# Optimization experiments

Hardware: AMD Instinct MI355X
Metric: run time of the kernel (lower is better)

The kernel has to match this reference:

```python
import jax, jax.numpy as jnp
import numpy as np

EMB = 1024
HEADS = 16
HEADSIZE = EMB // HEADS
EPS = 1e-5  # torch LayerNorm default


def _layernorm(x, g, b):
    # normalize over last dim (headsize)
    m = jnp.mean(x, axis=-1, keepdims=True)
    v = jnp.mean((x - m) ** 2, axis=-1, keepdims=True)
    return (x - m) * jax.lax.rsqrt(v + EPS) * g + b


def setup_inputs() -> dict:
    key = jax.random.key(0)
    ks = jax.random.split(key, 6)
    B, T = 4, 2048
    s = 1.0 / np.sqrt(EMB)  # ~ torch Linear init scale
    return {
        "x": jax.random.normal(ks[0], (B, T, EMB), dtype=jnp.float32),
        "Wk": jax.random.normal(ks[1], (EMB, EMB), dtype=jnp.float32) * s,
        "Wq": jax.random.normal(ks[2], (EMB, EMB), dtype=jnp.float32) * s,
        "Wv": jax.random.normal(ks[3], (EMB, EMB), dtype=jnp.float32) * s,
        "Wo": jax.random.normal(ks[4], (EMB, EMB), dtype=jnp.float32) * s,
        "bo": jnp.zeros((EMB,), dtype=jnp.float32),
        "kln_g": jnp.ones((HEADSIZE,), dtype=jnp.float32),
        "kln_b": jnp.zeros((HEADSIZE,), dtype=jnp.float32),
        "qln_g": jnp.ones((HEADSIZE,), dtype=jnp.float32),
        "qln_b": jnp.zeros((HEADSIZE,), dtype=jnp.float32),
    }


def reference(x, Wk, Wq, Wv, Wo, bo, kln_g, kln_b, qln_g, qln_b):
    B, T, E = x.shape
    # projections (torch Linear: y = x @ W.T), split into heads
    k = jnp.einsum("bte,fe->btf", x, Wk).reshape(B, T, HEADS, HEADSIZE)
    q = jnp.einsum("bte,fe->btf", x, Wq).reshape(B, T, HEADS, HEADSIZE)
    v = jnp.einsum("bte,fe->btf", x, Wv).reshape(B, T, HEADS, HEADSIZE)
    # optional per-head layernorm on keys/queries (kqnorm=True)
    k = _layernorm(k, kln_g, kln_b)
    q = _layernorm(q, qln_g, qln_b)
    # note: original scales by emb**-1/4 on each of q and k (total 1/sqrt(emb))
    scale = E ** (-0.25)
    q = q * scale
    k = k * scale
    # full [B, H, T, T] score matrix (faithful to bmm implementation)
    dot = jnp.einsum("bihd,bjhd->bhij", q, k)
    # causal mask: j > i set to -inf (mask_diagonal=False -> offset=1)
    causal = jnp.triu(jnp.ones((T, T), dtype=bool), k=1)
    dot = jnp.where(causal, -jnp.inf, dot)
    att = jax.nn.softmax(dot, axis=-1)
    out = jnp.einsum("bhij,bjhd->bihd", att, v).reshape(B, T, E)
    return jnp.einsum("bte,fe->btf", out, Wo) + bo
```

## Files before the change

### kernel.cpp

```cpp
#include <hip/hip_runtime.h>
#include <hip/hip_bf16.h>
#include <cstdint>

#define EMB 1024
#define HEADS 16
#define HD 64
#define BATCH 4
#define SEQ 2048
#define BT (BATCH*SEQ)
#define LNEPS 1e-5f
#define QK_SCALE 0.17677669529663687f
#define LOG2E 1.4426950408889634f

typedef __bf16 bf16;
typedef __bf16 bf16x8 __attribute__((ext_vector_type(8)));
typedef __bf16 bf16x4 __attribute__((ext_vector_type(4)));
typedef float  f32x4  __attribute__((ext_vector_type(4)));
typedef short  s16x4  __attribute__((ext_vector_type(4)));

typedef const __attribute__((address_space(1))) void* gas_ptr;
typedef __attribute__((address_space(3))) void*       las_ptr;

__device__ __forceinline__ void gld_lds16(const void* g, void* l) {
  __builtin_amdgcn_global_load_lds((gas_ptr)g, (las_ptr)l, 16, 0, 0);
}

__device__ __forceinline__ f32x4 mfma_pv(bf16x4 a, bf16x4 b, f32x4 c) {
  return __builtin_amdgcn_mfma_f32_16x16x16bf16_1k(
      __builtin_bit_cast(s16x4, a), __builtin_bit_cast(s16x4, b), c, 0, 0, 0);
}

__global__ void cvt_f32_bf16(const float* __restrict__ src, bf16* __restrict__ dst, int n4) {
  int i = blockIdx.x * blockDim.x + threadIdx.x;
  if (i >= n4) return;
  float4 f = reinterpret_cast<const float4*>(src)[i];
  bf16x4 o = { (bf16)f.x, (bf16)f.y, (bf16)f.z, (bf16)f.w };
  reinterpret_cast<bf16x4*>(dst)[i] = o;
}

__global__ void cvt_w4(const float* __restrict__ w0, const float* __restrict__ w1,
                       const float* __restrict__ w2, const float* __restrict__ w3,
                       bf16* __restrict__ dst) {
  int i = blockIdx.x * blockDim.x + threadIdx.x;
  int sel = i >> 18;
  int j = i & 262143;
  const float* s = (sel == 0) ? w0 : (sel == 1) ? w1 : (sel == 2) ? w2 : w3;
  float4 f = reinterpret_cast<const float4*>(s)[j];
  bf16x4 o = { (bf16)f.x, (bf16)f.y, (bf16)f.z, (bf16)f.w };
  reinterpret_cast<bf16x4*>(dst)[i] = o;
}

template<int OUTF32>
__global__ __launch_bounds__(256, 2) void gemm_bt(
    const bf16* __restrict__ A, const bf16* __restrict__ Bm,
    bf16* __restrict__ Cb, float* __restrict__ Cf, const float* __restrict__ bias,
    int M, int N, int K)
{
  __shared__ __align__(16) bf16 As[128 * 32];
  __shared__ __align__(16) bf16 Bs[128 * 32];

  const int t    = threadIdx.x;
  const int lane = t & 63;
  const int wave = t >> 6;
  const int q    = lane >> 4;
  const int ln   = lane & 15;
  const int m0   = blockIdx.y * 128;
  const int n0   = blockIdx.x * 128;
  const int wm   = (wave >> 1) * 64;
  const int wn   = (wave & 1) * 64;

  const int r0 = t >> 2;
  const int c0 = (t & 3) << 3;

  f32x4 zero4 = {0.f, 0.f, 0.f, 0.f};
  f32x4 acc[4][4];
#pragma unroll
  for (int i = 0; i < 4; i++)
#pragma unroll
    for (int j = 0; j < 4; j++) acc[i][j] = zero4;

  for (int k0 = 0; k0 < K; k0 += 32) {
    __syncthreads();
    const bf16* ga = A  + (size_t)(m0 + r0) * K + k0 + c0;
    const bf16* gb = Bm + (size_t)(n0 + r0) * K + k0 + c0;
    gld_lds16(ga,                  &As[t * 8]);
    gld_lds16(ga + (size_t)64 * K, &As[t * 8 + 2048]);
    gld_lds16(gb,                  &Bs[t * 8]);
    gld_lds16(gb + (size_t)64 * K, &Bs[t * 8 + 2048]);
    __syncthreads();

    bf16x8 af[4], bfr[4];
#pragma unroll
    for (int mi = 0; mi < 4; mi++)
      af[mi] = *reinterpret_cast<const bf16x8*>(&As[(wm + mi * 16 + ln) * 32 + q * 8]);
#pragma unroll
    for (int ni = 0; ni < 4; ni++)
      bfr[ni] = *reinterpret_cast<const bf16x8*>(&Bs[(wn + ni * 16 + ln) * 32 + q * 8]);
#pragma unroll
    for (int mi = 0; mi < 4; mi++)
#pragma unroll
      for (int ni = 0; ni < 4; ni++)
        acc[mi][ni] = __builtin_amdgcn_mfma_f32_16x16x32_bf16(af[mi], bfr[ni], acc[mi][ni], 0, 0, 0);
  }

#pragma unroll
  for (int mi = 0; mi < 4; mi++) {
#pragma unroll
    for (int ni = 0; ni < 4; ni++) {
#pragma unroll
      for (int r = 0; r < 4; r++) {
        int row = m0 + wm + mi * 16 + q * 4 + r;
        int col = n0 + wn + ni * 16 + ln;
        float v = acc[mi][ni][r];
        if (OUTF32) Cf[(size_t)row * N + col] = v + bias[col];
        else        Cb[(size_t)row * N + col] = (bf16)v;
      }
    }
  }
}

__global__ void ln_kq(const bf16* __restrict__ kqv,
                      bf16* __restrict__ kn, bf16* __restrict__ qn,
                      const float* __restrict__ kg, const float* __restrict__ kb,
                      const float* __restrict__ qg, const float* __restrict__ qb,
                      float kscale, float qscale)
{
  const int t = threadIdx.x;
  const int lr = t & 7;
  const int row = blockIdx.x * 32 + (t >> 3);
  const int tok = row >> 4, h = row & 15;
  const size_t base = (size_t)tok * (3 * EMB) + h * HD + lr * 8;

  bf16x8 vk = *reinterpret_cast<const bf16x8*>(kqv + base);
  bf16x8 vq = *reinterpret_cast<const bf16x8*>(kqv + base + EMB);

  float fk[8], fq[8];
  float sk = 0.f, sq = 0.f, s2k = 0.f, s2q = 0.f;
#pragma unroll
  for (int e = 0; e < 8; e++) {
    fk[e] = (float)vk[e]; fq[e] = (float)vq[e];
    sk += fk[e]; sq += fq[e];
    s2k += fk[e] * fk[e]; s2q += fq[e] * fq[e];
  }
#pragma unroll
  for (int m = 1; m < 8; m <<= 1) {
    sk  += __shfl_xor(sk,  m, 64); sq  += __shfl_xor(sq,  m, 64);
    s2k += __shfl_xor(s2k, m, 64); s2q += __shfl_xor(s2q, m, 64);
  }
  float mk = sk * (1.f / 64.f), mq = sq * (1.f / 64.f);
  float rk = rsqrtf(s2k * (1.f / 64.f) - mk * mk + LNEPS) * kscale;
  float rq = rsqrtf(s2q * (1.f / 64.f) - mq * mq + LNEPS) * qscale;

  bf16x8 ok, oq;
#pragma unroll
  for (int e = 0; e < 8; e++) {
    float gk = kg[lr * 8 + e], bk2 = kb[lr * 8 + e];
    float gq = qg[lr * 8 + e], bq2 = qb[lr * 8 + e];
    ok[e] = (bf16)(((fk[e] - mk) * rk) * gk + bk2 * kscale);
    oq[e] = (bf16)(((fq[e] - mq) * rq) * gq + bq2 * qscale);
  }
  const int b = tok >> 11, tt = tok & 2047;
  const size_t o = ((size_t)(b * HEADS + h) * SEQ + tt) * HD + lr * 8;
  *reinterpret_cast<bf16x8*>(kn + o) = ok;
  *reinterpret_cast<bf16x8*>(qn + o) = oq;
}

__global__ void v_trans(const bf16* __restrict__ in, int ldin, bf16* __restrict__ out)
{
  __shared__ __align__(16) bf16 tile[64][72];
  int bh = blockIdx.y, jt = blockIdx.x;
  int b = bh >> 4, h = bh & 15;
  int t = threadIdx.x;
#pragma unroll
  for (int p = 0; p < 2; p++) {
    int rowj = p * 32 + (t >> 3);
    int cold = (t & 7) << 3;
    bf16x8 v = *reinterpret_cast<const bf16x8*>(
        &in[(size_t)(b * SEQ + jt * 64 + rowj) * ldin + h * HD + cold]);
    *reinterpret_cast<bf16x8*>(&tile[rowj][cold]) = v;
  }
  __syncthreads();
#pragma unroll
  for (int p = 0; p < 2; p++) {
    int rowd = p * 32 + (t >> 3);
    int colj = (t & 7) << 3;
    bf16x8 v;
#pragma unroll
    for (int jj = 0; jj < 8; jj++) v[jj] = tile[colj + jj][rowd];
    *reinterpret_cast<bf16x8*>(&out[((size_t)bh * HD + rowd) * SEQ + jt * 64 + colj]) = v;
  }
}

__global__ __launch_bounds__(256, 8) void attn(
    const bf16* __restrict__ Qn, const bf16* __restrict__ Kn, const bf16* __restrict__ Vt,
    bf16* __restrict__ O)
{
  __shared__ __align__(16) bf16 Ks[32 * 64];
  __shared__ __align__(16) bf16 Vs[64 * 32];

  const int bh = blockIdx.y;
  const int itile = ((int)blockIdx.x + (int)blockIdx.y) & 31;
  const int i0 = itile * 64;
  const int t = threadIdx.x, wave = t >> 6, lane = t & 63;
  const int q = lane >> 4, ln = lane & 15;
  const int qbase = i0 + wave * 16;

  const bf16* qp = Qn + ((size_t)bh * SEQ + qbase + ln) * HD + q * 8;
  bf16x8 qf0 = *reinterpret_cast<const bf16x8*>(qp);
  bf16x8 qf1 = *reinterpret_cast<const bf16x8*>(qp + 32);

  float lrow = 0.f;
  f32x4 zero4 = {0.f, 0.f, 0.f, 0.f};
  f32x4 oacc[4];
#pragma unroll
  for (int md = 0; md < 4; md++) oacc[md] = zero4;

  const int nj = 2 * itile + 2;
  for (int jt = 0; jt < nj; jt++) {
    const int j0 = jt * 32;
    {
      const int u = t * 8;
      const int krow = u >> 6;
      const int kcs = (t & 7) ^ (krow & 7);
      gld_lds16(Kn + ((size_t)bh * SEQ + j0 + krow) * HD + kcs * 8, &Ks[u]);
      const int vd = u >> 5;
      const int vcs = (t & 3) ^ ((vd >> 1) & 3);
      gld_lds16(Vt + ((size_t)bh * HD + vd) * SEQ + j0 + vcs * 8, &Vs[u]);
    }
    __syncthreads();

#pragma unroll
    for (int jb = 0; jb < 2; jb++) {
      if ((j0 + jb * 16) <= (qbase + 15)) {
        const int rowj = jb * 16 + ln;
        bf16x8 kf0 = *reinterpret_cast<const bf16x8*>(&Ks[rowj * 64 + ((q)     ^ (rowj & 7)) * 8]);
        bf16x8 kf1 = *reinterpret_cast<const bf16x8*>(&Ks[rowj * 64 + ((4 + q) ^ (rowj & 7)) * 8]);
        f32x4 z = zero4;
        z = __builtin_amdgcn_mfma_f32_16x16x32_bf16(kf0, qf0, z, 0, 0, 0);
        z = __builtin_amdgcn_mfma_f32_16x16x32_bf16(kf1, qf1, z, 0, 0, 0);
        if (j0 + jb * 16 + 15 > qbase) {
#pragma unroll
          for (int r = 0; r < 4; r++) {
            int jj = j0 + jb * 16 + q * 4 + r;
            int ii = qbase + ln;
            if (jj > ii) z[r] = -1.0e30f;
          }
        }
        float p0 = exp2f(z[0]), p1 = exp2f(z[1]), p2 = exp2f(z[2]), p3 = exp2f(z[3]);
        lrow += (p0 + p1) + (p2 + p3);
        bf16x4 pk = { (bf16)p0, (bf16)p1, (bf16)p2, (bf16)p3 };

#pragma unroll
        for (int md = 0; md < 4; md++) {
          const int rowd = md * 16 + ln;
          const bf16* vp = &Vs[rowd * 32 + (((jb * 2 + (q >> 1)) ^ ((rowd >> 1) & 3)) * 8) + (q & 1) * 4];
          bf16x4 vf = *reinterpret_cast<const bf16x4*>(vp);
          oacc[md] = mfma_pv(vf, pk, oacc[md]);
        }
      }
    }
    __syncthreads();
  }

  float s = lrow;
  s += __shfl_xor(s, 16, 64);
  s += __shfl_xor(s, 32, 64);
  const float inv = 1.f / s;
  const int b = bh >> 4, h = bh & 15;
  const int row = qbase + ln;
#pragma unroll
  for (int md = 0; md < 4; md++) {
    bf16x4 o4 = { (bf16)(oacc[md][0] * inv), (bf16)(oacc[md][1] * inv),
                  (bf16)(oacc[md][2] * inv), (bf16)(oacc[md][3] * inv) };
    int col = h * HD + md * 16 + q * 4;
    *reinterpret_cast<bf16x4*>(&O[(size_t)(b * SEQ + row) * EMB + col]) = o4;
  }
}

extern "C" void kernel_launch(void* const* d_in, const int* in_sizes, int n_in,
                              void* d_out, int out_size, void* d_ws, size_t ws_size,
                              hipStream_t stream)
{
  const float* x   = (const float*)d_in[0];
  const float* Wk  = (const float*)d_in[1];
  const float* Wq  = (const float*)d_in[2];
  const float* Wv  = (const float*)d_in[3];
  const float* Wo  = (const float*)d_in[4];
  const float* bo  = (const float*)d_in[5];
  const float* klg = (const float*)d_in[6];
  const float* klb = (const float*)d_in[7];
  const float* qlg = (const float*)d_in[8];
  const float* qlb = (const float*)d_in[9];
  float* out = (float*)d_out;

  char* ws = (char*)d_ws;
  const size_t OFF_XB  = 0;
  const size_t OFF_WB  = OFF_XB  + (size_t)BT * EMB * 2;
  const size_t OFF_KQV = OFF_WB  + (size_t)4 * EMB * EMB * 2;
  const size_t OFF_KN  = OFF_KQV + (size_t)BT * 3 * EMB * 2;
  const size_t OFF_QN  = OFF_KN  + (size_t)BT * EMB * 2;
  const size_t OFF_VT  = OFF_QN  + (size_t)BT * EMB * 2;
  const size_t OFF_END = OFF_VT  + (size_t)BT * EMB * 2;
  if (ws_size < OFF_END) return;

  bf16* xb   = (bf16*)(ws + OFF_XB);
  bf16* wb   = (bf16*)(ws + OFF_WB);
  bf16* kqv  = (bf16*)(ws + OFF_KQV);
  bf16* kn   = (bf16*)(ws + OFF_KN);
  bf16* qn   = (bf16*)(ws + OFF_QN);
  bf16* vt   = (bf16*)(ws + OFF_VT);
  bf16* ob   = (bf16*)(ws + OFF_KQV);

  cvt_f32_bf16<<<(BT * EMB / 4) / 256, 256, 0, stream>>>(x, xb, BT * EMB / 4);
  cvt_w4<<<(4 * EMB * EMB / 4) / 256, 256, 0, stream>>>(Wk, Wq, Wv, Wo, wb);

  gemm_bt<0><<<dim3(3 * EMB / 128, BT / 128), 256, 0, stream>>>(
      xb, wb, kqv, (float*)nullptr, (const float*)nullptr, BT, 3 * EMB, EMB);

  ln_kq<<<BT * HEADS / 32, 256, 0, stream>>>(kqv, kn, qn, klg, klb, qlg, qlb,
                                             QK_SCALE * LOG2E, QK_SCALE);
  v_trans<<<dim3(SEQ / 64, BATCH * HEADS), 256, 0, stream>>>(kqv + 2 * EMB, 3 * EMB, vt);

  attn<<<dim3(32, BATCH * HEADS), 256, 0, stream>>>(qn, kn, vt, ob);

  gemm_bt<1><<<dim3(EMB / 128, BT / 128), 256, 0, stream>>>(
      ob, wb + (size_t)3 * EMB * EMB, (bf16*)nullptr, out, bo, BT, EMB, EMB);
}
```

Measured before the change: 312.3 us.

## Double-buffer K/V tiles and pair causal query tiles per attention block

The attention kernel now loads 64-key K/V tiles into double-buffered LDS, prefetching the next tile while computing on the current one, which removes one barrier per iteration. Each block handles two query tiles (itile and 31-itile) so work is balanced across blocks under the causal mask, and the grid is halved. This raises LDS use and lowers the occupancy hint from 8 to 4 blocks per CU, and the V swizzle is changed to fit the wider tile.

New measurement: 300.0 us. 1.04x faster.

```diff
diff --git a/kernel.cpp b/kernel.cpp
--- a/kernel.cpp
+++ b/kernel.cpp
@@ -191,89 +191,111 @@
   }
 }
 
-__global__ __launch_bounds__(256, 8) void attn(
+__global__ __launch_bounds__(256, 4) void attn(
     const bf16* __restrict__ Qn, const bf16* __restrict__ Kn, const bf16* __restrict__ Vt,
     bf16* __restrict__ O)
 {
-  __shared__ __align__(16) bf16 Ks[32 * 64];
-  __shared__ __align__(16) bf16 Vs[64 * 32];
+  __shared__ __align__(16) bf16 Ks[2][64 * 64];
+  __shared__ __align__(16) bf16 Vs[2][64 * 64];
 
   const int bh = blockIdx.y;
-  const int itile = ((int)blockIdx.x + (int)blockIdx.y) & 31;
-  const int i0 = itile * 64;
   const int t = threadIdx.x, wave = t >> 6, lane = t & 63;
   const int q = lane >> 4, ln = lane & 15;
-  const int qbase = i0 + wave * 16;
-
-  const bf16* qp = Qn + ((size_t)bh * SEQ + qbase + ln) * HD + q * 8;
-  bf16x8 qf0 = *reinterpret_cast<const bf16x8*>(qp);
-  bf16x8 qf1 = *reinterpret_cast<const bf16x8*>(qp + 32);
-
-  float lrow = 0.f;
+  const int b = bh >> 4, h = bh & 15;
+
+  const int u0 = t * 8, u1 = t * 8 + 2048;
+  const int kr0 = u0 >> 6, kc0 = ((u0 >> 3) & 7) ^ (kr0 & 7);
+  const int kr1 = u1 >> 6, kc1 = ((u1 >> 3) & 7) ^ (kr1 & 7);
+  const int vd0 = u0 >> 6, vc0 = ((u0 >> 3) & 7) ^ (vd0 & 7);
+  const int vd1 = u1 >> 6, vc1 = ((u1 >> 3) & 7) ^ (vd1 & 7);
+  const bf16* Kb = Kn + (size_t)bh * SEQ * HD;
+  const bf16* Vb = Vt + (size_t)bh * HD * SEQ;
+
   f32x4 zero4 = {0.f, 0.f, 0.f, 0.f};
-  f32x4 oacc[4];
-#pragma unroll
-  for (int md = 0; md < 4; md++) oacc[md] = zero4;
-
-  const int nj = 2 * itile + 2;
-  for (int jt = 0; jt < nj; jt++) {
-    const int j0 = jt * 32;
+
+  for (int pass = 0; pass < 2; ++pass) {
+    const int itile = pass ? (31 - (int)blockIdx.x) : (int)blockIdx.x;
+    const int qbase = itile * 64 + wave * 16;
+
+    const bf16* qp = Qn + ((size_t)bh * SEQ + qbase + ln) * HD + q * 8;
+    bf16x8 qf0 = *reinterpret_cast<const bf16x8*>(qp);
+    bf16x8 qf1 = *reinterpret_cast<const bf16x8*>(qp + 32);
+
+    float lrow = 0.f;
+    f32x4 oacc[4];
+#pragma unroll
+    for (int md = 0; md < 4; md++) oacc[md] = zero4;
+
+    const int nj = itile + 1;
+
+    __syncthreads();
     {
-      const int u = t * 8;
-      const int krow = u >> 6;
-      const int kcs = (t & 7) ^ (krow & 7);
-      gld_lds16(Kn + ((size_t)bh * SEQ + j0 + krow) * HD + kcs * 8, &Ks[u]);
-      const int vd = u >> 5;
-      const int vcs = (t & 3) ^ ((vd >> 1) & 3);
-      gld_lds16(Vt + ((size_t)bh * HD + vd) * SEQ + j0 + vcs * 8, &Vs[u]);
+      gld_lds16(Kb + (size_t)kr0 * HD + kc0 * 8, &Ks[0][u0]);
+      gld_lds16(Kb + (size_t)kr1 * HD + kc1 * 8, &Ks[0][u1]);
+      gld_lds16(Vb + (size_t)vd0 * SEQ + vc0 * 8, &Vs[0][u0]);
+      gld_lds16(Vb + (size_t)vd1 * SEQ + vc1 * 8, &Vs[0][u1]);
     }
-    __syncthreads();
-
-#pragma unroll
-    for (int jb = 0; jb < 2; jb++) {
-      if ((j0 + jb * 16) <= (qbase + 15)) {
-        const int rowj = jb * 16 + ln;
-        bf16x8 kf0 = *reinterpret_cast<const bf16x8*>(&Ks[rowj * 64 + ((q)     ^ (rowj & 7)) * 8]);
-        bf16x8 kf1 = *reinterpret_cast<const bf16x8*>(&Ks[rowj * 64 + ((4 + q) ^ (rowj & 7)) * 8]);
-        f32x4 z = zero4;
-        z = __builtin_amdgcn_mfma_f32_16x16x32_bf16(kf0, qf0, z, 0, 0, 0);
-        z = __builtin_amdgcn_mfma_f32_16x16x32_bf16(kf1, qf1, z, 0, 0, 0);
-        if (j0 + jb * 16 + 15 > qbase) {
-#pragma unroll
-          for (int r = 0; r < 4; r++) {
-            int jj = j0 + jb * 16 + q * 4 + r;
-            int ii = qbase + ln;
-            if (jj > ii) z[r] = -1.0e30f;
+
+    for (int jt = 0; jt < nj; ++jt) {
+      const int buf = jt & 1;
+      const int j0 = jt * 64;
+      __syncthreads();
+      if (jt + 1 < nj) {
+        const int jn = j0 + 64;
+        gld_lds16(Kb + (size_t)(jn + kr0) * HD + kc0 * 8, &Ks[buf ^ 1][u0]);
+        gld_lds16(Kb + (size_t)(jn + kr1) * HD + kc1 * 8, &Ks[buf ^ 1][u1]);
+        gld_lds16(Vb + (size_t)vd0 * SEQ + jn + vc0 * 8, &Vs[buf ^ 1][u0]);
+        gld_lds16(Vb + (size_t)vd1 * SEQ + jn + vc1 * 8, &Vs[buf ^ 1][u1]);
+      }
+
+#pragma unroll
+      for (int jb = 0; jb < 4; ++jb) {
+        const int jslab = j0 + jb * 16;
+        if (jslab <= qbase + 15) {
+          const int rowj = jb * 16 + ln;
+          bf16x8 kf0 = *reinterpret_cast<const bf16x8*>(
+              &Ks[buf][rowj * 64 + ((q)     ^ (rowj & 7)) * 8]);
+          bf16x8 kf1 = *reinterpret_cast<const bf16x8*>(
+              &Ks[buf][rowj * 64 + ((4 + q) ^ (rowj & 7)) * 8]);
+          f32x4 z = zero4;
+          z = __builtin_amdgcn_mfma_f32_16x16x32_bf16(kf0, qf0, z, 0, 0, 0);
+          z = __builtin_amdgcn_mfma_f32_16x16x32_bf16(kf1, qf1, z, 0, 0, 0);
+          if (jslab + 15 > qbase) {
+#pragma unroll
+            for (int r = 0; r < 4; r++) {
+              int jj = jslab + q * 4 + r;
+              int ii = qbase + ln;
+              if (jj > ii) z[r] = -1.0e30f;
+            }
           }
-        }
-        float p0 = exp2f(z[0]), p1 = exp2f(z[1]), p2 = exp2f(z[2]), p3 = exp2f(z[3]);
-        lrow += (p0 + p1) + (p2 + p3);
-        bf16x4 pk = { (bf16)p0, (bf16)p1, (bf16)p2, (bf16)p3 };
-
-#pragma unroll
-        for (int md = 0; md < 4; md++) {
-          const int rowd = md * 16 + ln;
-          const bf16* vp = &Vs[rowd * 32 + (((jb * 2 + (q >> 1)) ^ ((rowd >> 1) & 3)) * 8) + (q & 1) * 4];
-          bf16x4 vf = *reinterpret_cast<const bf16x4*>(vp);
-          oacc[md] = mfma_pv(vf, pk, oacc[md]);
+          float p0 = exp2f(z[0]), p1 = exp2f(z[1]), p2 = exp2f(z[2]), p3 = exp2f(z[3]);
+          lrow += (p0 + p1) + (p2 + p3);
+          bf16x4 pk = { (bf16)p0, (bf16)p1, (bf16)p2, (bf16)p3 };
+
+#pragma unroll
+          for (int md = 0; md < 4; md++) {
+            const int rowd = md * 16 + ln;
+            const bf16* vp = &Vs[buf][rowd * 64 +
+                (((jb * 2 + (q >> 1)) ^ (rowd & 7)) * 8) + (q & 1) * 4];
+            bf16x4 vf = *reinterpret_cast<const bf16x4*>(vp);
+            oacc[md] = mfma_pv(vf, pk, oacc[md]);
+          }
         }
       }
     }
-    __syncthreads();
-  }
-
-  float s = lrow;
-  s += __shfl_xor(s, 16, 64);
-  s += __shfl_xor(s, 32, 64);
-  const float inv = 1.f / s;
-  const int b = bh >> 4, h = bh & 15;
-  const int row = qbase + ln;
-#pragma unroll
-  for (int md = 0; md < 4; md++) {
-    bf16x4 o4 = { (bf16)(oacc[md][0] * inv), (bf16)(oacc[md][1] * inv),
-                  (bf16)(oacc[md][2] * inv), (bf16)(oacc[md][3] * inv) };
-    int col = h * HD + md * 16 + q * 4;
-    *reinterpret_cast<bf16x4*>(&O[(size_t)(b * SEQ + row) * EMB + col]) = o4;
+
+    float s = lrow;
+    s += __shfl_xor(s, 16, 64);
+    s += __shfl_xor(s, 32, 64);
+    const float inv = 1.f / s;
+    const int row = qbase + ln;
+#pragma unroll
+    for (int md = 0; md < 4; md++) {
+      bf16x4 o4 = { (bf16)(oacc[md][0] * inv), (bf16)(oacc[md][1] * inv),
+                    (bf16)(oacc[md][2] * inv), (bf16)(oacc[md][3] * inv) };
+      int col = h * HD + md * 16 + q * 4;
+      *reinterpret_cast<bf16x4*>(&O[(size_t)(b * SEQ + row) * EMB + col]) = o4;
+    }
   }
 }
 
@@ -321,7 +343,7 @@
                                              QK_SCALE * LOG2E, QK_SCALE);
   v_trans<<<dim3(SEQ / 64, BATCH * HEADS), 256, 0, stream>>>(kqv + 2 * EMB, 3 * EMB, vt);
 
-  attn<<<dim3(32, BATCH * HEADS), 256, 0, stream>>>(qn, kn, vt, ob);
+  attn<<<dim3(16, BATCH * HEADS), 256, 0, stream>>>(qn, kn, vt, ob);
 
   gemm_bt<1><<<dim3(EMB / 128, BT / 128), 256, 0, stream>>>(
       ob, wb + (size_t)3 * EMB * EMB, (bf16*)nullptr, out, bo, BT, EMB, EMB);
```
